# Kernel tuning notes

Measured on AMD Instinct MI355X. Metric: run time of the kernel, lower is better.

Reference implementation:

```python
import jax, jax.numpy as jnp
import numpy as np

N_NODES = 10000
N_EDGES = 320000
IN_FEATS = 512
N_UNITS = 256
OUT_FEATS = 64
N_LAYERS = 6  # number of hidden GCNConv layers feeding the JK max


def setup_inputs() -> dict:
    key = jax.random.key(0)
    ks = jax.random.split(key, 8)
    h = jax.random.normal(ks[0], (N_NODES, IN_FEATS), dtype=jnp.float32)
    edge_index = jax.random.randint(ks[1], (2, N_EDGES), 0, N_NODES, dtype=jnp.int64)
    # learned parameters (glorot-ish scale)
    W0 = jax.random.normal(ks[2], (IN_FEATS, N_UNITS), dtype=jnp.float32) * (1.0 / np.sqrt(IN_FEATS))
    b0 = jnp.zeros((N_UNITS,), dtype=jnp.float32)
    Wh = jax.random.normal(ks[3], (N_LAYERS - 1, N_UNITS, N_UNITS), dtype=jnp.float32) * (1.0 / np.sqrt(N_UNITS))
    bh = jnp.zeros((N_LAYERS - 1, N_UNITS), dtype=jnp.float32)
    Wo = jax.random.normal(ks[4], (N_UNITS, OUT_FEATS), dtype=jnp.float32) * (1.0 / np.sqrt(N_UNITS))
    bo = jnp.zeros((OUT_FEATS,), dtype=jnp.float32)
    return {"h": h, "edge_index": edge_index, "W0": W0, "b0": b0,
            "Wh": Wh, "bh": bh, "Wo": Wo, "bo": bo}


def reference(h, edge_index, W0, b0, Wh, bh, Wo, bo):
    src = edge_index[0]
    dst = edge_index[1]
    n = h.shape[0]

    def conv_plain(x, W, b):
        # GCNConv with normalize=False: plain sum aggregation over edges, no self-loops
        m = x @ W                                   # [N, d]
        agg = jax.ops.segment_sum(m[src], dst, num_segments=n)
        return jax.nn.relu(agg + b)

    outs = []
    x = conv_plain(h, W0, b0)
    outs.append(x)
    for i in range(Wh.shape[0]):  # dropout is identity in eval mode
        x = conv_plain(x, Wh[i], bh[i])
        outs.append(x)

    # jumping-knowledge max aggregation over layer outputs
    x = jnp.max(jnp.stack(outs, axis=0), axis=0)    # [N, n_units]

    # final GCNConv with normalize=True (symmetric GCN norm, self-loops added)
    m = x @ Wo                                      # [N, out_feats]
    ones = jnp.ones(dst.shape, dtype=m.dtype)
    deg = jax.ops.segment_sum(ones, dst, num_segments=n) + 1.0  # +1 self loop
    dinv = deg ** -0.5
    coef = dinv[src] * dinv[dst]                    # [E]
    agg = jax.ops.segment_sum(m[src] * coef[:, None], dst, num_segments=n)
    agg = agg + m / deg[:, None] + bo               # self-loop term 1/deg_i
    return jax.nn.log_softmax(agg, axis=-1)
```

## Files before the change

### kernel.cpp

```cpp
#include <hip/hip_runtime.h>
#include <math.h>

#define N_NODES 10000
#define N_EDGES 320000
#define IN_FEATS 512
#define N_UNITS 256
#define OUT_FEATS 64
#define N_HID 5

typedef __attribute__((ext_vector_type(8))) short bf16x8;
typedef __attribute__((ext_vector_type(4))) float f32x4;

__device__ __forceinline__ unsigned short f2bf(float f) {
    union { float f; unsigned int u; } c; c.f = f;
    unsigned int u = c.u + 0x7FFFu + ((c.u >> 16) & 1u);
    return (unsigned short)(u >> 16);
}
__device__ __forceinline__ float bf2f(unsigned int b) {
    union { unsigned int u; float f; } c; c.u = (b & 0xffffu) << 16;
    return c.f;
}


__global__ void k_setup(const int* __restrict__ dst, int* __restrict__ deg,
                        const float* __restrict__ h, unsigned short* __restrict__ hb,
                        const float* __restrict__ W0, const float* __restrict__ Wh,
                        const float* __restrict__ Wo,
                        unsigned short* __restrict__ W0t, unsigned short* __restrict__ Wht,
                        unsigned short* __restrict__ Wot) {
    const int R1 = N_EDGES;
    const int R2 = N_NODES * IN_FEATS / 4;
    const int S0 = IN_FEATS * N_UNITS;
    const int SH = N_HID * N_UNITS * N_UNITS;
    const int SO = N_UNITS * OUT_FEATS;
    int t = blockIdx.x * blockDim.x + threadIdx.x;
    if (t < R1) {
        atomicAdd(&deg[dst[t]], 1);
    } else if (t < R1 + R2) {
        int u = t - R1;
        float4 v = reinterpret_cast<const float4*>(h)[u];
        ushort4 o;
        o.x = f2bf(v.x); o.y = f2bf(v.y); o.z = f2bf(v.z); o.w = f2bf(v.w);
        reinterpret_cast<ushort4*>(hb)[u] = o;
    } else {
        int u = t - R1 - R2;
        if (u < S0) {
            int k = u >> 8, n = u & 255;
            W0t[(size_t)n * IN_FEATS + k] = f2bf(W0[u]);
        } else if (u < S0 + SH) {
            int w = u - S0;
            int l = w >> 16, r = w & 65535;
            int k = r >> 8, n = r & 255;
            Wht[(size_t)l * 65536 + (size_t)n * N_UNITS + k] = f2bf(Wh[w]);
        } else if (u < S0 + SH + SO) {
            int w = u - S0 - SH;
            int k = w >> 6, n = w & 63;
            Wot[(size_t)n * N_UNITS + k] = f2bf(Wo[w]);
        }
    }
}


__global__ __launch_bounds__(1024) void k_scan(const int* __restrict__ deg,
                                               int* __restrict__ row_ptr,
                                               int* __restrict__ cursor,
                                               float* __restrict__ dinv,
                                               float* __restrict__ invdeg) {
    __shared__ int wsum[16];
    const int PER = 10;
    int t = threadIdx.x;
    int lane = t & 63, wid = t >> 6;
    int base = t * PER;

    int v[PER];
    int s = 0;
#pragma unroll
    for (int j = 0; j < PER; ++j) {
        int i = base + j;
        int d = (i < N_NODES) ? deg[i] : 0;
        v[j] = s;
        s += d;
    }
    int inc = s;
#pragma unroll
    for (int off = 1; off < 64; off <<= 1) {
        int y = __shfl_up(inc, off);
        if (lane >= off) inc += y;
    }
    if (lane == 63) wsum[wid] = inc;
    __syncthreads();
    if (wid == 0) {
        int w = (lane < 16) ? wsum[lane] : 0;
#pragma unroll
        for (int off = 1; off < 16; off <<= 1) {
            int y = __shfl_up(w, off);
            if (lane >= off) w += y;
        }
        if (lane < 16) wsum[lane] = w;
    }
    __syncthreads();
    int wave_excl = (wid == 0) ? 0 : wsum[wid - 1];
    int thread_excl = wave_excl + (inc - s);

#pragma unroll
    for (int j = 0; j < PER; ++j) {
        int i = base + j;
        if (i < N_NODES) {
            int rp = thread_excl + v[j];
            row_ptr[i] = rp;
            cursor[i]  = rp;
            int d = ((j + 1 < PER) ? v[j + 1] : s) - v[j];
            float dd = (float)(d + 1);
            dinv[i]   = rsqrtf(dd);
            invdeg[i] = 1.0f / dd;
        }
    }
    if (t == 1023) row_ptr[N_NODES] = thread_excl + s;
}

__global__ void k_fill(const int* __restrict__ src, const int* __restrict__ dst,
                       int* __restrict__ cursor, int* __restrict__ csr_src) {
    int e = blockIdx.x * blockDim.x + threadIdx.x;
    if (e < N_EDGES) {
        int p = atomicAdd(&cursor[dst[e]], 1);
        csr_src[p] = src[e];
    }
}


__global__ __launch_bounds__(256) void k_mgemm(const unsigned short* __restrict__ A,
                                               const unsigned short* __restrict__ Bt,
                                               unsigned short* __restrict__ C,
                                               const int M, const int K, const int Nld) {
    constexpr int BM = 64, BN = 64, BK = 32;
    __shared__ unsigned short As[2][BM * BK];
    __shared__ unsigned short Bs[2][BN * BK];

    const int tid  = threadIdx.x;
    const int wid  = tid >> 6;
    const int lane = tid & 63;
    const int wr   = wid >> 1;
    const int wc   = wid & 1;
    const int brow = blockIdx.y * BM;
    const int bcol = blockIdx.x * BN;

    const int lr = lane & 15;
    const int lk = lane >> 4;

    const int row  = tid >> 2;
    const int slot = tid & 3;
    const int sslot = slot ^ ((row >> 1) & 3);

    int gra = brow + row; if (gra >= M) gra = M - 1;
    const unsigned short* gpa = A + (size_t)gra * K + sslot * 8;
    const unsigned short* gpb = Bt + (size_t)(bcol + row) * K + sslot * 8;

    f32x4 acc[2][2];
#pragma unroll
    for (int m = 0; m < 2; ++m)
#pragma unroll
        for (int n = 0; n < 2; ++n)
            acc[m][n] = (f32x4){0.f, 0.f, 0.f, 0.f};

#define STAGE(buf, k0)                                                                      \
    do {                                                                                    \
        __builtin_amdgcn_global_load_lds(                                                   \
            (const __attribute__((address_space(1))) void*)(gpa + (k0)),                    \
            (__attribute__((address_space(3))) void*)(&As[(buf)][tid * 8]), 16, 0, 0);      \
        __builtin_amdgcn_global_load_lds(                                                   \
            (const __attribute__((address_space(1))) void*)(gpb + (k0)),                    \
            (__attribute__((address_space(3))) void*)(&Bs[(buf)][tid * 8]), 16, 0, 0);      \
    } while (0)

    STAGE(0, 0);
    __syncthreads();

    const int nk = K / BK;
    for (int kt = 0; kt < nk; ++kt) {
        const int cur = kt & 1;
        if (kt + 1 < nk) STAGE(cur ^ 1, (kt + 1) * BK);

        bf16x8 af[2], bfr[2];
#pragma unroll
        for (int m = 0; m < 2; ++m) {
            int ra = wr * 32 + m * 16 + lr;
            af[m] = *reinterpret_cast<const bf16x8*>(&As[cur][ra * BK + (lk ^ ((ra >> 1) & 3)) * 8]);
        }
#pragma unroll
        for (int n = 0; n < 2; ++n) {
            int rb = wc * 32 + n * 16 + lr;
            bfr[n] = *reinterpret_cast<const bf16x8*>(&Bs[cur][rb * BK + (lk ^ ((rb >> 1) & 3)) * 8]);
        }
#pragma unroll
        for (int m = 0; m < 2; ++m)
#pragma unroll
            for (int n = 0; n < 2; ++n)
                acc[m][n] = __builtin_amdgcn_mfma_f32_16x16x32_bf16(af[m], bfr[n], acc[m][n], 0, 0, 0);
        __syncthreads();
    }
#undef STAGE

#pragma unroll
    for (int m = 0; m < 2; ++m) {
#pragma unroll
        for (int r = 0; r < 4; ++r) {
            int orow = brow + wr * 32 + m * 16 + lk * 4 + r;
            if (orow < M) {
#pragma unroll
                for (int n = 0; n < 2; ++n) {
                    int ocol = bcol + wc * 32 + n * 16 + lr;
                    C[(size_t)orow * Nld + ocol] = f2bf(acc[m][n][r]);
                }
            }
        }
    }
}


__global__ __launch_bounds__(256) void k_wgemm(const unsigned short* __restrict__ A,
                                               const unsigned short* __restrict__ Bt,
                                               unsigned short* __restrict__ C,
                                               const int M, const int Nld) {
    constexpr int K = 256;
    __shared__ unsigned short As[64 * K];
    __shared__ unsigned short Bs[64 * K];

    const int tid  = threadIdx.x;
    const int wid  = tid >> 6;
    const int lane = tid & 63;
    const int lr   = lane & 15;
    const int lk   = lane >> 4;
    const int brow = blockIdx.y * 64;
    const int bcol = blockIdx.x * 64;

#pragma unroll
    for (int p = 0; p < 8; ++p) {
        int i = p * 256 + tid;
        int row = i >> 5, s = i & 31;
        int gr = brow + row; if (gr >= M) gr = M - 1;
        const unsigned short* gp = A + (size_t)gr * K + ((s ^ (row & 7)) * 8);
        __builtin_amdgcn_global_load_lds(
            (const __attribute__((address_space(1))) void*)gp,
            (__attribute__((address_space(3))) void*)(As + i * 8), 16, 0, 0);
    }
#pragma unroll
    for (int p = 0; p < 8; ++p) {
        int i = p * 256 + tid;
        int row = i >> 5, s = i & 31;
        const unsigned short* gp = Bt + (size_t)(bcol + row) * K + ((s ^ (row & 7)) * 8);
        __builtin_amdgcn_global_load_lds(
            (const __attribute__((address_space(1))) void*)gp,
            (__attribute__((address_space(3))) void*)(Bs + i * 8), 16, 0, 0);
    }
    __syncthreads();

    f32x4 acc[4];
#pragma unroll
    for (int n = 0; n < 4; ++n) acc[n] = (f32x4){0.f, 0.f, 0.f, 0.f};

    const int ra = (wid << 4) + lr;
    const unsigned short* Arow = As + ra * K;
    const int e = lr & 7;
#pragma unroll
    for (int kk = 0; kk < 8; ++kk) {
        bf16x8 av = *reinterpret_cast<const bf16x8*>(&Arow[(((kk << 2) + lk) ^ e) * 8]);
#pragma unroll
        for (int n = 0; n < 4; ++n) {
            const unsigned short* Brow = Bs + ((n << 4) + lr) * K;
            bf16x8 bv = *reinterpret_cast<const bf16x8*>(&Brow[(((kk << 2) + lk) ^ e) * 8]);
            acc[n] = __builtin_amdgcn_mfma_f32_16x16x32_bf16(av, bv, acc[n], 0, 0, 0);
        }
    }

#pragma unroll
    for (int n = 0; n < 4; ++n) {
#pragma unroll
        for (int r = 0; r < 4; ++r) {
            int orow = brow + (wid << 4) + (lk << 2) + r;
            if (orow < M) {
                int ocol = bcol + (n << 4) + lr;
                C[(size_t)orow * Nld + ocol] = f2bf(acc[n][r]);
            }
        }
    }
}


__global__ __launch_bounds__(256) void k_agg(const unsigned short* __restrict__ m,
                                             const int* __restrict__ row_ptr,
                                             const int* __restrict__ csr_src,
                                             const float* __restrict__ bias,
                                             unsigned short* __restrict__ x_out,
                                             unsigned short* __restrict__ jk,
                                             int init_jk) {
    const int halfsel = (blockIdx.x >= 625) ? 1 : 0;
    const int g = blockIdx.x - halfsel * 625;
    const int nib  = threadIdx.x >> 4;
    const int lane = threadIdx.x & 15;
    const int n = g * 16 + nib;
    const int s = row_ptr[n], e = row_ptr[n + 1];
    const uint4* mv = (const uint4*)m;
    const int off = halfsel * 16 + lane;

    float a[8];
#pragma unroll
    for (int j = 0; j < 8; ++j) a[j] = 0.f;

#define ACC8(u)                                        \
    do {                                               \
        a[0] += bf2f((u).x); a[1] += bf2f((u).x >> 16);\
        a[2] += bf2f((u).y); a[3] += bf2f((u).y >> 16);\
        a[4] += bf2f((u).z); a[5] += bf2f((u).z >> 16);\
        a[6] += bf2f((u).w); a[7] += bf2f((u).w >> 16);\
    } while (0)

    int i = s;
    for (; i + 3 < e; i += 4) {
        int s0 = csr_src[i], s1 = csr_src[i + 1], s2 = csr_src[i + 2], s3 = csr_src[i + 3];
        uint4 u0 = mv[(size_t)s0 * 32 + off];
        uint4 u1 = mv[(size_t)s1 * 32 + off];
        uint4 u2 = mv[(size_t)s2 * 32 + off];
        uint4 u3 = mv[(size_t)s3 * 32 + off];
        ACC8(u0); ACC8(u1); ACC8(u2); ACC8(u3);
    }
    for (; i < e; ++i) {
        uint4 u = mv[(size_t)csr_src[i] * 32 + off];
        ACC8(u);
    }
#undef ACC8

    float4 b0 = ((const float4*)bias)[halfsel * 32 + lane * 2];
    float4 b1 = ((const float4*)bias)[halfsel * 32 + lane * 2 + 1];
    unsigned int hh[8];
    hh[0] = f2bf(fmaxf(a[0] + b0.x, 0.f));
    hh[1] = f2bf(fmaxf(a[1] + b0.y, 0.f));
    hh[2] = f2bf(fmaxf(a[2] + b0.z, 0.f));
    hh[3] = f2bf(fmaxf(a[3] + b0.w, 0.f));
    hh[4] = f2bf(fmaxf(a[4] + b1.x, 0.f));
    hh[5] = f2bf(fmaxf(a[5] + b1.y, 0.f));
    hh[6] = f2bf(fmaxf(a[6] + b1.z, 0.f));
    hh[7] = f2bf(fmaxf(a[7] + b1.w, 0.f));
    uint4 o;
    o.x = hh[0] | (hh[1] << 16);
    o.y = hh[2] | (hh[3] << 16);
    o.z = hh[4] | (hh[5] << 16);
    o.w = hh[6] | (hh[7] << 16);

    size_t idx = (size_t)n * 32 + off;
    ((uint4*)x_out)[idx] = o;
    if (init_jk) {
        ((uint4*)jk)[idx] = o;
    } else {
        uint4 j = ((const uint4*)jk)[idx];
        auto mx2 = [](unsigned int nw, unsigned int od) {
            unsigned int lo_n = nw & 0xffffu, lo_o = od & 0xffffu;
            unsigned int hi_n = nw >> 16,     hi_o = od >> 16;
            unsigned int lo = lo_n > lo_o ? lo_n : lo_o;
            unsigned int hi = hi_n > hi_o ? hi_n : hi_o;
            return lo | (hi << 16);
        };
        uint4 w;
        w.x = mx2(o.x, j.x); w.y = mx2(o.y, j.y);
        w.z = mx2(o.z, j.z); w.w = mx2(o.w, j.w);
        ((uint4*)jk)[idx] = w;
    }
}


__global__ __launch_bounds__(256) void k_final(const unsigned short* __restrict__ mf,
                                               const int* __restrict__ row_ptr,
                                               const int* __restrict__ csr_src,
                                               const float* __restrict__ dinv,
                                               const float* __restrict__ invdeg,
                                               const float* __restrict__ bo,
                                               float* __restrict__ out) {
    int halfw = threadIdx.x >> 5;
    int wl = threadIdx.x & 31;
    const unsigned int* mfu = (const unsigned int*)mf;
    int n = blockIdx.x * 8 + halfw;
    int s = row_ptr[n], e = row_ptr[n + 1];

    float a0 = 0.f, a1 = 0.f;
    int i = s;
    for (; i + 1 < e; i += 2) {
        int s0 = csr_src[i], s1 = csr_src[i + 1];
        unsigned int u0 = mfu[(size_t)s0 * 32 + wl];
        unsigned int u1 = mfu[(size_t)s1 * 32 + wl];
        float d0 = dinv[s0], d1 = dinv[s1];
        a0 += bf2f(u0) * d0 + bf2f(u1) * d1;
        a1 += bf2f(u0 >> 16) * d0 + bf2f(u1 >> 16) * d1;
    }
    for (; i < e; ++i) {
        int sr = csr_src[i];
        unsigned int u = mfu[(size_t)sr * 32 + wl];
        float dv = dinv[sr];
        a0 += bf2f(u) * dv;
        a1 += bf2f(u >> 16) * dv;
    }
    float dn = dinv[n];
    a0 *= dn; a1 *= dn;
    unsigned int un = mfu[(size_t)n * 32 + wl];
    float idg = invdeg[n];
    float2 bo2 = ((const float2*)bo)[wl];
    a0 += bf2f(un) * idg + bo2.x;
    a1 += bf2f(un >> 16) * idg + bo2.y;

    float mx = fmaxf(a0, a1);
#pragma unroll
    for (int off = 16; off; off >>= 1) mx = fmaxf(mx, __shfl_xor(mx, off));
    float e0 = __expf(a0 - mx), e1 = __expf(a1 - mx);
    float sum = e0 + e1;
#pragma unroll
    for (int off = 16; off; off >>= 1) sum += __shfl_xor(sum, off);
    float ls = __logf(sum);
    float2 r;
    r.x = a0 - mx - ls;
    r.y = a1 - mx - ls;
    ((float2*)out)[(size_t)n * 32 + wl] = r;
}


extern "C" void kernel_launch(void* const* d_in, const int* in_sizes, int n_in,
                              void* d_out, int out_size, void* d_ws, size_t ws_size,
                              hipStream_t stream) {
    const float* h  = (const float*)d_in[0];
    const int*   ei = (const int*)d_in[1];
    const float* W0 = (const float*)d_in[2];
    const float* b0 = (const float*)d_in[3];
    const float* Wh = (const float*)d_in[4];
    const float* bh = (const float*)d_in[5];
    const float* Wo = (const float*)d_in[6];
    const float* bo = (const float*)d_in[7];

    const int* src = ei;
    const int* dst = ei + N_EDGES;

    char* p = (char*)d_ws;
    auto carve = [&](size_t bytes) {
        char* r = p;
        p += (bytes + 255) & ~(size_t)255;
        return r;
    };
    int*   deg     = (int*)  carve(N_NODES * 4);
    int*   row_ptr = (int*)  carve((N_NODES + 1) * 4);
    int*   cursor  = (int*)  carve(N_NODES * 4);
    int*   csr_src = (int*)  carve(N_EDGES * 4);
    float* dinv    = (float*)carve(N_NODES * 4);
    float* invdeg  = (float*)carve(N_NODES * 4);
    unsigned short* hb  = (unsigned short*)carve((size_t)N_NODES * IN_FEATS * 2);
    unsigned short* W0t = (unsigned short*)carve((size_t)IN_FEATS * N_UNITS * 2);
    unsigned short* Wht = (unsigned short*)carve((size_t)N_HID * N_UNITS * N_UNITS * 2);
    unsigned short* Wot = (unsigned short*)carve((size_t)N_UNITS * OUT_FEATS * 2);
    unsigned short* m   = (unsigned short*)carve((size_t)N_NODES * N_UNITS * 2);
    unsigned short* x   = (unsigned short*)carve((size_t)N_NODES * N_UNITS * 2);
    unsigned short* jk  = (unsigned short*)carve((size_t)N_NODES * N_UNITS * 2);
    unsigned short* mf  = (unsigned short*)carve((size_t)N_NODES * OUT_FEATS * 2);

    hipMemsetAsync(deg, 0, N_NODES * 4, stream);
    {
        const int total = N_EDGES + N_NODES * IN_FEATS / 4 +
                          IN_FEATS * N_UNITS + N_HID * N_UNITS * N_UNITS + N_UNITS * OUT_FEATS;
        k_setup<<<(total + 255) / 256, 256, 0, stream>>>(dst, deg, h, hb, W0, Wh, Wo,
                                                         W0t, Wht, Wot);
    }
    k_scan<<<1, 1024, 0, stream>>>(deg, row_ptr, cursor, dinv, invdeg);
    k_fill<<<(N_EDGES + 255) / 256, 256, 0, stream>>>(src, dst, cursor, csr_src);

    const int GBM = (N_NODES + 63) / 64;

    {
        dim3 g(N_UNITS / 64, GBM);
        k_mgemm<<<g, 256, 0, stream>>>(hb, W0t, m, N_NODES, IN_FEATS, N_UNITS);
    }
    k_agg<<<1250, 256, 0, stream>>>(m, row_ptr, csr_src, b0, x, jk, 1);

    for (int l = 0; l < N_HID; ++l) {
        dim3 g(N_UNITS / 64, GBM);
        k_wgemm<<<g, 256, 0, stream>>>(x, Wht + (size_t)l * N_UNITS * N_UNITS, m,
                                       N_NODES, N_UNITS);
        k_agg<<<1250, 256, 0, stream>>>(m, row_ptr, csr_src, bh + (size_t)l * N_UNITS,
                                        x, jk, 0);
    }

    {
        dim3 g(OUT_FEATS / 64, GBM);
        k_wgemm<<<g, 256, 0, stream>>>(jk, Wot, mf, N_NODES, OUT_FEATS);
    }
    k_final<<<N_NODES / 8, 256, 0, stream>>>(mf, row_ptr, csr_src, dinv, invdeg,
                                             bo, (float*)d_out);
}
```

Measured before the change: 262.6 us.

## Fuse hidden-layer aggregation with weight GEMM by aggregating before multiplying

Each hidden layer now computes (A·X)·W instead of A·(X·W). One kernel gathers neighbour features for 16 nodes into LDS, then multiplies by W with MFMA, adding bias, ReLU and the JK max in its epilogue. This removes the separate GEMM launch and the round trip of the intermediate m buffer through global memory, and ping-pongs between two x buffers. In exchange, every block reloads the full 256x256 weight matrix, the MFMA tiles are only 16 rows tall, LDS use per block is high, and the epilogue writes 2-byte values column-wise. The aggregated sum is also rounded to bf16 before the GEMM.

```diff
diff --git a/kernel.cpp b/kernel.cpp
--- a/kernel.cpp
+++ b/kernel.cpp
@@ -217,82 +217,12 @@
 }
 
 
-__global__ __launch_bounds__(256) void k_wgemm(const unsigned short* __restrict__ A,
-                                               const unsigned short* __restrict__ Bt,
-                                               unsigned short* __restrict__ C,
-                                               const int M, const int Nld) {
-    constexpr int K = 256;
-    __shared__ unsigned short As[64 * K];
-    __shared__ unsigned short Bs[64 * K];
-
-    const int tid  = threadIdx.x;
-    const int wid  = tid >> 6;
-    const int lane = tid & 63;
-    const int lr   = lane & 15;
-    const int lk   = lane >> 4;
-    const int brow = blockIdx.y * 64;
-    const int bcol = blockIdx.x * 64;
-
-#pragma unroll
-    for (int p = 0; p < 8; ++p) {
-        int i = p * 256 + tid;
-        int row = i >> 5, s = i & 31;
-        int gr = brow + row; if (gr >= M) gr = M - 1;
-        const unsigned short* gp = A + (size_t)gr * K + ((s ^ (row & 7)) * 8);
-        __builtin_amdgcn_global_load_lds(
-            (const __attribute__((address_space(1))) void*)gp,
-            (__attribute__((address_space(3))) void*)(As + i * 8), 16, 0, 0);
-    }
-#pragma unroll
-    for (int p = 0; p < 8; ++p) {
-        int i = p * 256 + tid;
-        int row = i >> 5, s = i & 31;
-        const unsigned short* gp = Bt + (size_t)(bcol + row) * K + ((s ^ (row & 7)) * 8);
-        __builtin_amdgcn_global_load_lds(
-            (const __attribute__((address_space(1))) void*)gp,
-            (__attribute__((address_space(3))) void*)(Bs + i * 8), 16, 0, 0);
-    }
-    __syncthreads();
-
-    f32x4 acc[4];
-#pragma unroll
-    for (int n = 0; n < 4; ++n) acc[n] = (f32x4){0.f, 0.f, 0.f, 0.f};
-
-    const int ra = (wid << 4) + lr;
-    const unsigned short* Arow = As + ra * K;
-    const int e = lr & 7;
-#pragma unroll
-    for (int kk = 0; kk < 8; ++kk) {
-        bf16x8 av = *reinterpret_cast<const bf16x8*>(&Arow[(((kk << 2) + lk) ^ e) * 8]);
-#pragma unroll
-        for (int n = 0; n < 4; ++n) {
-            const unsigned short* Brow = Bs + ((n << 4) + lr) * K;
-            bf16x8 bv = *reinterpret_cast<const bf16x8*>(&Brow[(((kk << 2) + lk) ^ e) * 8]);
-            acc[n] = __builtin_amdgcn_mfma_f32_16x16x32_bf16(av, bv, acc[n], 0, 0, 0);
-        }
-    }
-
-#pragma unroll
-    for (int n = 0; n < 4; ++n) {
-#pragma unroll
-        for (int r = 0; r < 4; ++r) {
-            int orow = brow + (wid << 4) + (lk << 2) + r;
-            if (orow < M) {
-                int ocol = bcol + (n << 4) + lr;
-                C[(size_t)orow * Nld + ocol] = f2bf(acc[n][r]);
-            }
-        }
-    }
-}
-
-
-__global__ __launch_bounds__(256) void k_agg(const unsigned short* __restrict__ m,
-                                             const int* __restrict__ row_ptr,
-                                             const int* __restrict__ csr_src,
-                                             const float* __restrict__ bias,
-                                             unsigned short* __restrict__ x_out,
-                                             unsigned short* __restrict__ jk,
-                                             int init_jk) {
+__global__ __launch_bounds__(256) void k_agg0(const unsigned short* __restrict__ m,
+                                              const int* __restrict__ row_ptr,
+                                              const int* __restrict__ csr_src,
+                                              const float* __restrict__ bias,
+                                              unsigned short* __restrict__ x_out,
+                                              unsigned short* __restrict__ jk) {
     const int halfsel = (blockIdx.x >= 625) ? 1 : 0;
     const int g = blockIdx.x - halfsel * 625;
     const int nib  = threadIdx.x >> 4;
@@ -348,21 +278,176 @@
 
     size_t idx = (size_t)n * 32 + off;
     ((uint4*)x_out)[idx] = o;
-    if (init_jk) {
-        ((uint4*)jk)[idx] = o;
-    } else {
-        uint4 j = ((const uint4*)jk)[idx];
-        auto mx2 = [](unsigned int nw, unsigned int od) {
-            unsigned int lo_n = nw & 0xffffu, lo_o = od & 0xffffu;
-            unsigned int hi_n = nw >> 16,     hi_o = od >> 16;
-            unsigned int lo = lo_n > lo_o ? lo_n : lo_o;
-            unsigned int hi = hi_n > hi_o ? hi_n : hi_o;
-            return lo | (hi << 16);
-        };
-        uint4 w;
-        w.x = mx2(o.x, j.x); w.y = mx2(o.y, j.y);
-        w.z = mx2(o.z, j.z); w.w = mx2(o.w, j.w);
-        ((uint4*)jk)[idx] = w;
+    ((uint4*)jk)[idx] = o;
+}
+
+
+__global__ __launch_bounds__(256) void k_lh16(const unsigned short* __restrict__ x_in,
+                                              const int* __restrict__ row_ptr,
+                                              const int* __restrict__ csr_src,
+                                              const unsigned short* __restrict__ Wt,
+                                              const float* __restrict__ bias,
+                                              unsigned short* __restrict__ x_out,
+                                              unsigned short* __restrict__ jk) {
+    constexpr int K = N_UNITS;
+    __shared__ unsigned short U[16 * K];
+    __shared__ unsigned short Bs[64 * K];
+
+    const int tid = threadIdx.x;
+    const int r = tid >> 4, sl = tid & 15;
+    const int n = blockIdx.x * 16 + r;
+    const int s = row_ptr[n], e = row_ptr[n + 1];
+    const uint4* xv = (const uint4*)x_in;
+
+    float a[16];
+#pragma unroll
+    for (int j = 0; j < 16; ++j) a[j] = 0.f;
+
+#define ACCL(u, base)                                                        \
+    do {                                                                     \
+        a[base + 0] += bf2f((u).x); a[base + 1] += bf2f((u).x >> 16);        \
+        a[base + 2] += bf2f((u).y); a[base + 3] += bf2f((u).y >> 16);        \
+        a[base + 4] += bf2f((u).z); a[base + 5] += bf2f((u).z >> 16);        \
+        a[base + 6] += bf2f((u).w); a[base + 7] += bf2f((u).w >> 16);        \
+    } while (0)
+
+    int i = s;
+    for (; i + 1 < e; i += 2) {
+        int s0 = csr_src[i], s1 = csr_src[i + 1];
+        uint4 u0 = xv[(size_t)s0 * 32 + sl];
+        uint4 u1 = xv[(size_t)s0 * 32 + 16 + sl];
+        uint4 u2 = xv[(size_t)s1 * 32 + sl];
+        uint4 u3 = xv[(size_t)s1 * 32 + 16 + sl];
+        ACCL(u0, 0); ACCL(u1, 8); ACCL(u2, 0); ACCL(u3, 8);
+    }
+    for (; i < e; ++i) {
+        int sr = csr_src[i];
+        uint4 u0 = xv[(size_t)sr * 32 + sl];
+        uint4 u1 = xv[(size_t)sr * 32 + 16 + sl];
+        ACCL(u0, 0); ACCL(u1, 8);
+    }
+#undef ACCL
+
+    uint4 o0, o1;
+    o0.x = f2bf(a[0])  | ((unsigned)f2bf(a[1])  << 16);
+    o0.y = f2bf(a[2])  | ((unsigned)f2bf(a[3])  << 16);
+    o0.z = f2bf(a[4])  | ((unsigned)f2bf(a[5])  << 16);
+    o0.w = f2bf(a[6])  | ((unsigned)f2bf(a[7])  << 16);
+    o1.x = f2bf(a[8])  | ((unsigned)f2bf(a[9])  << 16);
+    o1.y = f2bf(a[10]) | ((unsigned)f2bf(a[11]) << 16);
+    o1.z = f2bf(a[12]) | ((unsigned)f2bf(a[13]) << 16);
+    o1.w = f2bf(a[14]) | ((unsigned)f2bf(a[15]) << 16);
+    ((uint4*)U)[r * 32 + (sl ^ (r & 7))] = o0;
+    ((uint4*)U)[r * 32 + ((sl + 16) ^ (r & 7))] = o1;
+    __syncthreads();
+
+    const int wid = tid >> 6, lane = tid & 63;
+    const int lr = lane & 15, lk = lane >> 4;
+    const unsigned short* Urow = U + lr * K;
+    const int ex = lr & 7;
+
+    for (int ct = 0; ct < 4; ++ct) {
+#pragma unroll
+        for (int p = 0; p < 8; ++p) {
+            int i2 = p * 256 + tid;
+            int row = i2 >> 5, sx = i2 & 31;
+            const unsigned short* gp = Wt + (size_t)(ct * 64 + row) * K + ((sx ^ (row & 7)) * 8);
+            __builtin_amdgcn_global_load_lds(
+                (const __attribute__((address_space(1))) void*)gp,
+                (__attribute__((address_space(3))) void*)(Bs + i2 * 8), 16, 0, 0);
+        }
+        __syncthreads();
+
+        f32x4 acc = (f32x4){0.f, 0.f, 0.f, 0.f};
+        const unsigned short* Brow = Bs + (wid * 16 + lr) * K;
+#pragma unroll
+        for (int kk = 0; kk < 8; ++kk) {
+            bf16x8 av = *(const bf16x8*)(Urow + (((kk << 2) + lk) ^ ex) * 8);
+            bf16x8 bv = *(const bf16x8*)(Brow + (((kk << 2) + lk) ^ ex) * 8);
+            acc = __builtin_amdgcn_mfma_f32_16x16x32_bf16(av, bv, acc, 0, 0, 0);
+        }
+
+        int col = ct * 64 + wid * 16 + lr;
+        float bb = bias[col];
+#pragma unroll
+        for (int rr = 0; rr < 4; ++rr) {
+            int node = blockIdx.x * 16 + (lk << 2) + rr;
+            unsigned short v = f2bf(fmaxf(acc[rr] + bb, 0.f));
+            size_t idx = (size_t)node * N_UNITS + col;
+            x_out[idx] = v;
+            unsigned short jm = jk[idx];
+            jk[idx] = (v > jm) ? v : jm;
+        }
+        __syncthreads();
+    }
+}
+
+
+__global__ __launch_bounds__(256) void k_wgemm(const unsigned short* __restrict__ A,
+                                               const unsigned short* __restrict__ Bt,
+                                               unsigned short* __restrict__ C,
+                                               const int M, const int Nld) {
+    constexpr int K = 256;
+    __shared__ unsigned short As[64 * K];
+    __shared__ unsigned short Bs[64 * K];
+
+    const int tid  = threadIdx.x;
+    const int wid  = tid >> 6;
+    const int lane = tid & 63;
+    const int lr   = lane & 15;
+    const int lk   = lane >> 4;
+    const int brow = blockIdx.x * 64;
+    const int bcol = 0;
+
+#pragma unroll
+    for (int p = 0; p < 8; ++p) {
+        int i = p * 256 + tid;
+        int row = i >> 5, s = i & 31;
+        int gr = brow + row; if (gr >= M) gr = M - 1;
+        const unsigned short* gp = A + (size_t)gr * K + ((s ^ (row & 7)) * 8);
+        __builtin_amdgcn_global_load_lds(
+            (const __attribute__((address_space(1))) void*)gp,
+            (__attribute__((address_space(3))) void*)(As + i * 8), 16, 0, 0);
+    }
+#pragma unroll
+    for (int p = 0; p < 8; ++p) {
+        int i = p * 256 + tid;
+        int row = i >> 5, s = i & 31;
+        const unsigned short* gp = Bt + (size_t)(bcol + row) * K + ((s ^ (row & 7)) * 8);
+        __builtin_amdgcn_global_load_lds(
+            (const __attribute__((address_space(1))) void*)gp,
+            (__attribute__((address_space(3))) void*)(Bs + i * 8), 16, 0, 0);
+    }
+    __syncthreads();
+
+    f32x4 acc[4];
+#pragma unroll
+    for (int n = 0; n < 4; ++n) acc[n] = (f32x4){0.f, 0.f, 0.f, 0.f};
+
+    const int ra = (wid << 4) + lr;
+    const unsigned short* Arow = As + ra * K;
+    const int e = lr & 7;
+#pragma unroll
+    for (int kk = 0; kk < 8; ++kk) {
+        bf16x8 av = *reinterpret_cast<const bf16x8*>(&Arow[(((kk << 2) + lk) ^ e) * 8]);
+#pragma unroll
+        for (int n = 0; n < 4; ++n) {
+            const unsigned short* Brow = Bs + ((n << 4) + lr) * K;
+            bf16x8 bv = *reinterpret_cast<const bf16x8*>(&Brow[(((kk << 2) + lk) ^ e) * 8]);
+            acc[n] = __builtin_amdgcn_mfma_f32_16x16x32_bf16(av, bv, acc[n], 0, 0, 0);
+        }
+    }
+
+#pragma unroll
+    for (int n = 0; n < 4; ++n) {
+#pragma unroll
+        for (int r = 0; r < 4; ++r) {
+            int orow = brow + (wid << 4) + (lk << 2) + r;
+            if (orow < M) {
+                int ocol = bcol + (n << 4) + lr;
+                C[(size_t)orow * Nld + ocol] = f2bf(acc[n][r]);
+            }
+        }
     }
 }
 
@@ -452,7 +537,8 @@
     unsigned short* Wht = (unsigned short*)carve((size_t)N_HID * N_UNITS * N_UNITS * 2);
     unsigned short* Wot = (unsigned short*)carve((size_t)N_UNITS * OUT_FEATS * 2);
     unsigned short* m   = (unsigned short*)carve((size_t)N_NODES * N_UNITS * 2);
-    unsigned short* x   = (unsigned short*)carve((size_t)N_NODES * N_UNITS * 2);
+    unsigned short* xa  = (unsigned short*)carve((size_t)N_NODES * N_UNITS * 2);
+    unsigned short* xb  = (unsigned short*)carve((size_t)N_NODES * N_UNITS * 2);
     unsigned short* jk  = (unsigned short*)carve((size_t)N_NODES * N_UNITS * 2);
     unsigned short* mf  = (unsigned short*)carve((size_t)N_NODES * OUT_FEATS * 2);
 
@@ -472,20 +558,18 @@
         dim3 g(N_UNITS / 64, GBM);
         k_mgemm<<<g, 256, 0, stream>>>(hb, W0t, m, N_NODES, IN_FEATS, N_UNITS);
     }
-    k_agg<<<1250, 256, 0, stream>>>(m, row_ptr, csr_src, b0, x, jk, 1);
-
+    k_agg0<<<1250, 256, 0, stream>>>(m, row_ptr, csr_src, b0, xa, jk);
+
+    unsigned short* cur = xa;
+    unsigned short* nxt = xb;
     for (int l = 0; l < N_HID; ++l) {
-        dim3 g(N_UNITS / 64, GBM);
-        k_wgemm<<<g, 256, 0, stream>>>(x, Wht + (size_t)l * N_UNITS * N_UNITS, m,
-                                       N_NODES, N_UNITS);
-        k_agg<<<1250, 256, 0, stream>>>(m, row_ptr, csr_src, bh + (size_t)l * N_UNITS,
-                                        x, jk, 0);
-    }
-
-    {
-        dim3 g(OUT_FEATS / 64, GBM);
-        k_wgemm<<<g, 256, 0, stream>>>(jk, Wot, mf, N_NODES, OUT_FEATS);
-    }
+        k_lh16<<<625, 256, 0, stream>>>(cur, row_ptr, csr_src,
+                                        Wht + (size_t)l * N_UNITS * N_UNITS,
+                                        bh + (size_t)l * N_UNITS, nxt, jk);
+        unsigned short* t = cur; cur = nxt; nxt = t;
+    }
+
+    k_wgemm<<<GBM, 256, 0, stream>>>(jk, Wot, mf, N_NODES, OUT_FEATS);
     k_final<<<N_NODES / 8, 256, 0, stream>>>(mf, row_ptr, csr_src, dinv, invdeg,
                                              bo, (float*)d_out);
 }
```

Measured after the change: 270.5 us. 3.0% more time.
